# Kernel optimization log

Hardware: AMD Instinct MI355X
Metric: run time of the kernel (lower is better)

The kernel has to match this reference:

```python
import jax, jax.numpy as jnp
import numpy as np

# ---- static config (matches init_kwargs) ----
N, E = 8192, 262144
IN_CH, MP_CH, HID, K = 128, 512, 256, 10
EPS, DELTA = 1e-3, 0.311
TV_COEFF, BAL_COEFF = 0.785, 0.514


def setup_inputs() -> dict:
    key = jax.random.key(0)
    ks = jax.random.split(key, 16)

    def p(k, shape):
        fan_in = shape[0] if len(shape) > 1 else shape[0]
        return (jax.random.normal(k, shape, jnp.float32) / np.sqrt(fan_in)).astype(jnp.float32)

    return {
        "x": jax.random.normal(ks[0], (N, IN_CH), jnp.float32),
        "edge_index": jax.random.randint(ks[1], (2, E), 0, N, jnp.int32),
        "edge_weight": jax.random.uniform(ks[2], (E,), jnp.float32),
        # GTVConv layer 1 / 2 (Linear weight + bias)
        "W1": p(ks[3], (IN_CH, MP_CH)), "b1": jnp.zeros((MP_CH,), jnp.float32),
        "W2": p(ks[4], (MP_CH, MP_CH)), "b2": jnp.zeros((MP_CH,), jnp.float32),
        # pooling MLP [512 -> 256 -> K], relu, no norm
        "Wm1": p(ks[5], (MP_CH, HID)), "bm1": jnp.zeros((HID,), jnp.float32),
        "Wm2": p(ks[6], (HID, K)), "bm2": jnp.zeros((K,), jnp.float32),
    }


def _gtv_conv(x, src, dst, w, W, b):
    """GTVConv: out = elu( h - delta*(D_G h - Gamma h) + b ),
    gamma_ij = w_ij / max(||h_i - h_j||_1, eps), h = x @ W."""
    h = x @ W                                   # [N, C]
    diff = jnp.sum(jnp.abs(h[src] - h[dst]), axis=-1)   # [E]
    gamma = w / jnp.maximum(diff, EPS)                  # [E]
    deg = jnp.zeros(h.shape[0], h.dtype).at[dst].add(gamma)          # [N]
    agg = jnp.zeros_like(h).at[dst].add(gamma[:, None] * h[src])     # Gamma @ h
    out = h - DELTA * (deg[:, None] * h - agg) + b
    return jax.nn.elu(out)


def reference(x, edge_index, edge_weight, W1, b1, W2, b2, Wm1, bm1, Wm2, bm2):
    src, dst = edge_index[0], edge_index[1]

    h = _gtv_conv(x, src, dst, edge_weight, W1, b1)
    h = _gtv_conv(h, src, dst, edge_weight, W2, b2)

    # pooling MLP -> cluster logits s
    s_logits = jax.nn.relu(h @ Wm1 + bm1) @ Wm2 + bm2   # [N, K]

    # dense adjacency (to_dense_adj: duplicate edges accumulate)
    adj = jnp.zeros((N, N), x.dtype).at[src, dst].add(edge_weight)

    s = jax.nn.softmax(s_logits, axis=-1)

    # total-variation loss: sum_ij a_ij * sum_k |s_ik - s_jk| / (2 * nnz(adj))
    tv = jnp.zeros((), x.dtype)
    for k in range(K):  # small fixed loop over clusters, avoids [N,N,K] tensor
        col = s[:, k]
        tv = tv + jnp.sum(adj * jnp.abs(col[:, None] - col[None, :]))
    n_edges = jax.lax.stop_gradient(jnp.count_nonzero(adj).astype(x.dtype))
    tv = tv / (2.0 * n_edges)

    # asymmetric-norm balance loss (AsymCheegerCut)
    idx = N // K + 1                         # rho-quantile index (static)
    quant = jnp.sort(s, axis=0)[N - idx]     # idx-th largest per cluster, [K]
    t = s - quant[None, :]
    asym = jnp.where(t >= 0, (K - 1) * t, -t)
    denom = float(N * (K - 1))
    bal = (denom - jnp.sum(asym)) / denom

    return s_logits, TV_COEFF * tv, BAL_COEFF * bal
```

## Files before the change

kernel.cpp:

```cpp
#include <hip/hip_runtime.h>

#define N_NODES 8192
#define N_EDGES 262144
#define IN_CH 128
#define MP_CH 512
#define HID 256
#define KCL 10
#define EPS_C 0.001f
#define DELTA_C 0.311f
#define TV_COEFF_C 0.785f
#define BAL_COEFF_C 0.514f
#define RANK1 7373
#define DBINS 80


typedef __bf16 bf16x8 __attribute__((ext_vector_type(8)));
typedef float f32x4 __attribute__((ext_vector_type(4)));
typedef unsigned short ushort8 __attribute__((ext_vector_type(8)));

__device__ __forceinline__ float bf2f(unsigned short h) {
  union { unsigned int u; float f; } c; c.u = ((unsigned int)h) << 16; return c.f;
}
__device__ __forceinline__ unsigned short f2bf(float f) {
  union { float f; unsigned int u; } c; c.f = f;
  unsigned int r = c.u + 0x7fffu + ((c.u >> 16) & 1u);
  return (unsigned short)(r >> 16);
}

template <int CTRL, int RMASK>
__device__ __forceinline__ float dpp_add(float x) {
  int d = __builtin_amdgcn_update_dpp(0, __float_as_int(x), CTRL, RMASK, 0xf, true);
  return x + __int_as_float(d);
}
__device__ __forceinline__ float wave_sum64(float x) {
  x = dpp_add<0x111, 0xf>(x);
  x = dpp_add<0x112, 0xf>(x);
  x = dpp_add<0x114, 0xf>(x);
  x = dpp_add<0x118, 0xf>(x);
  x = dpp_add<0x142, 0xa>(x);
  x = dpp_add<0x143, 0xc>(x);
  return __int_as_float(__builtin_amdgcn_readlane(__float_as_int(x), 63));
}

__global__ void prep_kernel(const float* __restrict__ x, const float* __restrict__ W1,
                            const float* __restrict__ W2, const float* __restrict__ Wm1,
                            unsigned short* __restrict__ xb, unsigned short* __restrict__ W1bt,
                            unsigned short* __restrict__ W2bt, unsigned short* __restrict__ Wm1bt,
                            const int* __restrict__ dst, int* __restrict__ cnt) {
  int i = blockIdx.x * 256 + threadIdx.x;
  if (i < 131072) {
    f32x4 a = *(const f32x4*)(x + (size_t)i * 8);
    f32x4 b = *(const f32x4*)(x + (size_t)i * 8 + 4);
    ushort8 ov;
#pragma unroll
    for (int j = 0; j < 4; ++j) { ov[j] = f2bf(a[j]); ov[4 + j] = f2bf(b[j]); }
    *(ushort8*)(xb + (size_t)i * 8) = ov;
    return;
  }
  i -= 131072;
  if (i < 8192) {
    int n = i >> 4, kb = (i & 15) * 8;
    ushort8 ov;
#pragma unroll
    for (int r = 0; r < 8; ++r) ov[r] = f2bf(W1[(size_t)(kb + r) * MP_CH + n]);
    *(ushort8*)(W1bt + (size_t)i * 8) = ov;
    return;
  }
  i -= 8192;
  if (i < 32768) {
    int n = i >> 6, kb = (i & 63) * 8;
    ushort8 ov;
#pragma unroll
    for (int r = 0; r < 8; ++r) ov[r] = f2bf(W2[(size_t)(kb + r) * MP_CH + n]);
    *(ushort8*)(W2bt + (size_t)i * 8) = ov;
    return;
  }
  i -= 32768;
  if (i < 16384) {
    int n = i >> 6, kb = (i & 63) * 8;
    ushort8 ov;
#pragma unroll
    for (int r = 0; r < 8; ++r) ov[r] = f2bf(Wm1[(size_t)(kb + r) * HID + n]);
    *(ushort8*)(Wm1bt + (size_t)i * 8) = ov;
    return;
  }
  i -= 16384;
  if (i < N_EDGES) atomicAdd(&cnt[dst[i]], 1);
}

__global__ __launch_bounds__(1024) void scan_kernel(const int* __restrict__ cnt,
                                                    int* __restrict__ offs,
                                                    int* __restrict__ cursor,
                                                    int* __restrict__ nodeorder) {
  __shared__ int ts[1024];
  __shared__ int dh[DBINS];
  int t = threadIdx.x;
  int v[8]; int s = 0;
#pragma unroll
  for (int j = 0; j < 8; ++j) { v[j] = cnt[t * 8 + j]; s += v[j]; }
  if (t < DBINS) dh[t] = 0;
  ts[t] = s; __syncthreads();
  for (int off = 1; off < 1024; off <<= 1) {
    int add = (t >= off) ? ts[t - off] : 0;
    __syncthreads();
    ts[t] += add;
    __syncthreads();
  }
  int base = ts[t] - s;
#pragma unroll
  for (int j = 0; j < 8; ++j) {
    offs[t * 8 + j] = base; cursor[t * 8 + j] = base; base += v[j];
    int key = v[j] < (DBINS - 1) ? v[j] : (DBINS - 1);
    atomicAdd(&dh[(DBINS - 1) - key], 1);
  }
  if (t == 1023) offs[N_NODES] = ts[1023];
  __syncthreads();
  if (t == 0) {
    int acc0 = 0;
    for (int b = 0; b < DBINS; ++b) { int c = dh[b]; dh[b] = acc0; acc0 += c; }
  }
  __syncthreads();
#pragma unroll
  for (int j = 0; j < 8; ++j) {
    int key = v[j] < (DBINS - 1) ? v[j] : (DBINS - 1);
    int pos = atomicAdd(&dh[(DBINS - 1) - key], 1);
    nodeorder[pos] = t * 8 + j;
  }
}

__global__ void fill_kernel(const int* __restrict__ src, const int* __restrict__ dst,
                            const float* __restrict__ ew, int* __restrict__ cursor,
                            int2* __restrict__ esw, unsigned int* __restrict__ bitmap) {
  for (int e = blockIdx.x * blockDim.x + threadIdx.x; e < N_EDGES; e += gridDim.x * blockDim.x) {
    int a = src[e], b = dst[e];
    float w = ew[e];
    int p = atomicAdd(&cursor[b], 1);
    esw[p] = make_int2(a, __float_as_int(w));
    if (w != 0.f) {
      unsigned int key = ((unsigned int)a << 13) | (unsigned int)b;
      atomicOr(&bitmap[key >> 5], 1u << (key & 31u));
    }
  }
}

__global__ __launch_bounds__(256) void gemm_bt(
    const unsigned short* __restrict__ A, const unsigned short* __restrict__ BT,
    unsigned short* __restrict__ Cb, int N, int K) {
  __shared__ unsigned short lsm[2 * 128 * 32];
  unsigned short* lA = lsm;
  unsigned short* lB = lsm + 128 * 32;
  int lane = threadIdx.x & 63;
  int wv = threadIdx.x >> 6;
  int tm = blockIdx.y * 128, tn = blockIdx.x * 128;
  int wm = (wv >> 1) * 64, wn = (wv & 1) * 64;
  int rA = lane & 15, quad = lane >> 4;
  f32x4 acc[4][4];
#pragma unroll
  for (int i = 0; i < 4; ++i)
#pragma unroll
    for (int j = 0; j < 4; ++j) acc[i][j] = (f32x4){0.f, 0.f, 0.f, 0.f};

  int arow = wv * 32 + (lane >> 2);
  int acol = (lane & 3) * 8;

  for (int k0 = 0; k0 < K; k0 += 32) {
#pragma unroll
    for (int c = 0; c < 2; ++c) {
      const unsigned short* ga = A + (size_t)(tm + arow + c * 16) * K + k0 + acol;
      __builtin_amdgcn_global_load_lds(
          (const __attribute__((address_space(1))) unsigned int*)ga,
          (__attribute__((address_space(3))) unsigned int*)(lA + (wv * 32 + c * 16) * 32),
          16, 0, 0);
      const unsigned short* gb = BT + (size_t)(tn + arow + c * 16) * K + k0 + acol;
      __builtin_amdgcn_global_load_lds(
          (const __attribute__((address_space(1))) unsigned int*)gb,
          (__attribute__((address_space(3))) unsigned int*)(lB + (wv * 32 + c * 16) * 32),
          16, 0, 0);
    }
    __syncthreads();
    bf16x8 af[4], bfr[4];
#pragma unroll
    for (int i = 0; i < 4; ++i)
      af[i] = *(const bf16x8*)(lA + (wm + i * 16 + rA) * 32 + quad * 8);
#pragma unroll
    for (int j = 0; j < 4; ++j)
      bfr[j] = *(const bf16x8*)(lB + (wn + j * 16 + rA) * 32 + quad * 8);
#pragma unroll
    for (int i = 0; i < 4; ++i)
#pragma unroll
      for (int j = 0; j < 4; ++j)
        acc[i][j] = __builtin_amdgcn_mfma_f32_16x16x32_bf16(af[i], bfr[j], acc[i][j], 0, 0, 0);
    __syncthreads();
  }

  float* fbuf = (float*)lsm;
  int band = threadIdx.x >> 7;
  int rrow = (threadIdx.x >> 3) & 15;
  int cg = threadIdx.x & 7;
#pragma unroll
  for (int i = 0; i < 4; ++i) {
#pragma unroll
    for (int j = 0; j < 4; ++j)
#pragma unroll
      for (int r = 0; r < 4; ++r)
        fbuf[(wv >> 1) * (16 * 128) + (quad * 4 + r) * 128 + (wn + j * 16 + rA)] =
            acc[i][j][r];
    __syncthreads();
    const float* sr = fbuf + band * (16 * 128) + rrow * 128 + cg * 16;
    unsigned short ov[16];
#pragma unroll
    for (int c = 0; c < 16; ++c) ov[c] = f2bf(sr[c]);
    size_t gbase = (size_t)(tm + band * 64 + i * 16 + rrow) * N + tn + cg * 16;
    *(ushort8*)(Cb + gbase) = *(ushort8*)ov;
    *(ushort8*)(Cb + gbase + 8) = *(ushort8*)(ov + 8);
    __syncthreads();
  }
}

__global__ __launch_bounds__(256, 8) void gtv_node(
    const unsigned short* __restrict__ hb, const float* __restrict__ bias,
    const int2* __restrict__ esw, const int* __restrict__ offs,
    const int* __restrict__ nodeorder, unsigned short* __restrict__ outb) {
  __shared__ float sacc[2][MP_CH];
  int lane = threadIdx.x & 63;
  int wv = threadIdx.x >> 6;
  int pair = wv >> 1;
  int half = wv & 1;
  int d = __builtin_amdgcn_readfirstlane(nodeorder[blockIdx.x * 2 + pair]);
  ushort8 hdv = ((const ushort8*)(hb + (size_t)d * MP_CH))[lane];
  float hd[8], acc[8];
#pragma unroll
  for (int j = 0; j < 8; ++j) { hd[j] = bf2f(hdv[j]); acc[j] = 0.f; }
  int n0 = offs[d], n1 = offs[d + 1];
  int mid = n0 + ((n1 - n0 + 1) >> 1);
  int e0 = half ? mid : n0;
  int e1 = half ? n1 : mid;
  int i = e0;
  for (; i + 1 < e1; i += 2) {
    int2 ma = esw[i], mb = esw[i + 1];
    float wa = __int_as_float(ma.y), wb = __int_as_float(mb.y);
    ushort8 va = ((const ushort8*)(hb + (size_t)ma.x * MP_CH))[lane];
    ushort8 vb = ((const ushort8*)(hb + (size_t)mb.x * MP_CH))[lane];
    float pa = 0.f, pb = 0.f;
#pragma unroll
    for (int j = 0; j < 8; ++j) {
      pa += fabsf(hd[j] - bf2f(va[j]));
      pb += fabsf(hd[j] - bf2f(vb[j]));
    }
    pa = wave_sum64(pa);
    pb = wave_sum64(pb);
    float ga = wa * __builtin_amdgcn_rcpf(fmaxf(pa, EPS_C));
    float gb = wb * __builtin_amdgcn_rcpf(fmaxf(pb, EPS_C));
#pragma unroll
    for (int j = 0; j < 8; ++j)
      acc[j] += ga * (hd[j] - bf2f(va[j])) + gb * (hd[j] - bf2f(vb[j]));
  }
  if (i < e1) {
    int2 m0 = esw[i];
    float w = __int_as_float(m0.y);
    ushort8 sv = ((const ushort8*)(hb + (size_t)m0.x * MP_CH))[lane];
    float part = 0.f;
#pragma unroll
    for (int j = 0; j < 8; ++j) part += fabsf(hd[j] - bf2f(sv[j]));
    part = wave_sum64(part);
    float g = w * __builtin_amdgcn_rcpf(fmaxf(part, EPS_C));
#pragma unroll
    for (int j = 0; j < 8; ++j) acc[j] += g * (hd[j] - bf2f(sv[j]));
  }
  if (half) {
#pragma unroll
    for (int j = 0; j < 8; ++j) sacc[pair][lane * 8 + j] = acc[j];
  }
  __syncthreads();
  if (!half) {
    const f32x4* br = (const f32x4*)(bias + lane * 8);
    f32x4 b0 = br[0], b1 = br[1];
    unsigned short ov[8];
#pragma unroll
    for (int j = 0; j < 8; ++j) {
      float tot = acc[j] + sacc[pair][lane * 8 + j];
      float bv = (j < 4) ? b0[j] : b1[j - 4];
      float o = hd[j] - DELTA_C * tot + bv;
      o = (o > 0.f) ? o : (expf(o) - 1.f);
      ov[j] = f2bf(o);
    }
    *((ushort8*)(outb + (size_t)d * MP_CH) + lane) = *(ushort8*)ov;
  }
}

__global__ __launch_bounds__(256) void head_fused(
    const unsigned short* __restrict__ A,
    const unsigned short* __restrict__ BT,
    const float* __restrict__ bm1v, const float* __restrict__ Wm2v,
    const float* __restrict__ bm2v, float* __restrict__ out, float* __restrict__ s) {
  __shared__ unsigned short lA[32 * 32];
  __shared__ unsigned short lB[256 * 32];
  __shared__ float hbuf[256 * 41];
  __shared__ float lW2[HID * KCL];
  __shared__ float lb1[HID];
  __shared__ float lb2[KCL];
  int t = threadIdx.x;
  int lane = t & 63, wv = t >> 6;
  int rA = lane & 15, quad = lane >> 4;
  int m0 = blockIdx.x * 32;

  for (int i2 = t; i2 < HID * KCL; i2 += 256) lW2[i2] = Wm2v[i2];
  lb1[t < HID ? t : 0] = bm1v[t < HID ? t : 0];
  if (t < KCL) lb2[t] = bm2v[t];

  f32x4 acc[2][4];
#pragma unroll
  for (int i = 0; i < 2; ++i)
#pragma unroll
    for (int j = 0; j < 4; ++j) acc[i][j] = (f32x4){0.f, 0.f, 0.f, 0.f};

  for (int k0 = 0; k0 < MP_CH; k0 += 32) {
    if (wv < 2) {
      int row = wv * 16 + (lane >> 2);
      const unsigned short* ga = A + (size_t)(m0 + row) * MP_CH + k0 + (lane & 3) * 8;
      __builtin_amdgcn_global_load_lds(
          (const __attribute__((address_space(1))) unsigned int*)ga,
          (__attribute__((address_space(3))) unsigned int*)(lA + (wv * 16) * 32), 16, 0, 0);
    }
#pragma unroll
    for (int q = 0; q < 4; ++q) {
      int idx = wv * 4 + q;
      int row = idx * 16 + (lane >> 2);
      const unsigned short* gb = BT + (size_t)row * MP_CH + k0 + (lane & 3) * 8;
      __builtin_amdgcn_global_load_lds(
          (const __attribute__((address_space(1))) unsigned int*)gb,
          (__attribute__((address_space(3))) unsigned int*)(lB + (idx * 16) * 32), 16, 0, 0);
    }
    __syncthreads();
    bf16x8 af[2], bfr[4];
#pragma unroll
    for (int i = 0; i < 2; ++i)
      af[i] = *(const bf16x8*)(lA + (i * 16 + rA) * 32 + quad * 8);
#pragma unroll
    for (int j = 0; j < 4; ++j)
      bfr[j] = *(const bf16x8*)(lB + (wv * 64 + j * 16 + rA) * 32 + quad * 8);
#pragma unroll
    for (int i = 0; i < 2; ++i)
#pragma unroll
      for (int j = 0; j < 4; ++j)
        acc[i][j] = __builtin_amdgcn_mfma_f32_16x16x32_bf16(af[i], bfr[j], acc[i][j], 0, 0, 0);
    __syncthreads();
  }

#pragma unroll
  for (int i = 0; i < 2; ++i)
#pragma unroll
    for (int j = 0; j < 4; ++j)
#pragma unroll
      for (int r = 0; r < 4; ++r) {
        int row = i * 16 + quad * 4 + r;
        int col = wv * 64 + j * 16 + rA;
        hbuf[col * 41 + row] = fmaxf(acc[i][j][r] + lb1[col], 0.f);
      }
  __syncthreads();

  int row = t >> 3, g = t & 7;
  float p[KCL];
#pragma unroll
  for (int n = 0; n < KCL; ++n) p[n] = 0.f;
#pragma unroll
  for (int k = 0; k < 32; ++k) {
    int col = k * 8 + g;
    float hv = hbuf[col * 41 + row];
    const float* wr = lW2 + col * KCL;
#pragma unroll
    for (int n = 0; n < KCL; ++n) p[n] += hv * wr[n];
  }
#pragma unroll
  for (int n = 0; n < KCL; ++n) {
    p[n] += __shfl_xor(p[n], 1, 64);
    p[n] += __shfl_xor(p[n], 2, 64);
    p[n] += __shfl_xor(p[n], 4, 64);
  }
  if (g == 0) {
    float vv[KCL]; float mx = -1e30f;
    size_t gr = (size_t)(m0 + row);
#pragma unroll
    for (int n = 0; n < KCL; ++n) {
      vv[n] = p[n] + lb2[n];
      out[gr * KCL + n] = vv[n];
      mx = fmaxf(mx, vv[n]);
    }
    float sum = 0.f;
#pragma unroll
    for (int n = 0; n < KCL; ++n) { vv[n] = expf(vv[n] - mx); sum += vv[n]; }
    float inv = 1.f / sum;
#pragma unroll
    for (int n = 0; n < KCL; ++n) s[gr * KCL + n] = vv[n] * inv;
  }
}

__global__ __launch_bounds__(1024) void tvquant_kernel(
    const int* __restrict__ src, const int* __restrict__ dst,
    const float* __restrict__ ew, const float* __restrict__ s,
    const unsigned int* __restrict__ bitmap, float* __restrict__ scal,
    float* __restrict__ out) {
  __shared__ float fsh[16];
  __shared__ int wcnt[2][16];
  __shared__ int psh[16];
  int t = threadIdx.x;
  int lane = t & 63, wv = t >> 6;

  int local_pc = 0;
  {
    const uint4* bm4 = (const uint4*)(bitmap + (size_t)blockIdx.x * 8192);
    uint4 w0 = bm4[t * 2], w1 = bm4[t * 2 + 1];
    local_pc = __popc(w0.x) + __popc(w0.y) + __popc(w0.z) + __popc(w0.w) +
               __popc(w1.x) + __popc(w1.y) + __popc(w1.z) + __popc(w1.w);
  }

  if (blockIdx.x < 246) {
    float local = 0.f;
    for (int e = blockIdx.x * 1024 + t; e < N_EDGES; e += 246 * 1024) {
      int a = src[e], b = dst[e];
      float w = ew[e];
      const float* sa = s + (size_t)a * KCL;
      const float* sb = s + (size_t)b * KCL;
      float tv = 0.f;
#pragma unroll
      for (int k = 0; k < KCL; ++k) tv += fabsf(sa[k] - sb[k]);
      local += w * tv;
    }
#pragma unroll
    for (int m = 1; m < 64; m <<= 1) local += __shfl_xor(local, m, 64);
    if (lane == 0) fsh[wv] = local;
    __syncthreads();
    if (t == 0) {
      float tot = 0.f;
#pragma unroll
      for (int i2 = 0; i2 < 16; ++i2) tot += fsh[i2];
      atomicAdd(&scal[0], tot);
    }
  } else {
    int k = blockIdx.x - 246;
    unsigned int v[8];
#pragma unroll
    for (int j = 0; j < 8; ++j)
      v[j] = __float_as_uint(s[(size_t)(t + j * 1024) * KCL + k]);
    unsigned int lo = 0u, hi = 0x3F800000u;
    int p = 0;
    while (lo < hi) {
      unsigned int mid = (lo + hi) >> 1;
      int c = 0;
#pragma unroll
      for (int j = 0; j < 8; ++j) c += (v[j] <= mid) ? 1 : 0;
#pragma unroll
      for (int m = 1; m < 64; m <<= 1) c += __shfl_xor(c, m, 64);
      if (lane == 0) wcnt[p][wv] = c;
      __syncthreads();
      int tot = 0;
#pragma unroll
      for (int i2 = 0; i2 < 16; ++i2) tot += wcnt[p][i2];
      if (tot >= RANK1) hi = mid; else lo = mid + 1;
      p ^= 1;
    }
    float q = __uint_as_float(lo);
    float local = 0.f;
#pragma unroll
    for (int j = 0; j < 8; ++j) {
      float tt = __uint_as_float(v[j]) - q;
      local += (tt >= 0.f) ? 9.f * tt : -tt;
    }
#pragma unroll
    for (int m = 1; m < 64; m <<= 1) local += __shfl_xor(local, m, 64);
    if (lane == 0) fsh[wv] = local;
    __syncthreads();
    if (t == 0) {
      float tot = 0.f;
#pragma unroll
      for (int i2 = 0; i2 < 16; ++i2) tot += fsh[i2];
      atomicAdd(&scal[1], tot);
    }
  }

#pragma unroll
  for (int m = 1; m < 64; m <<= 1) local_pc += __shfl_xor(local_pc, m, 64);
  if (lane == 0) psh[wv] = local_pc;
  __syncthreads();
  if (t == 0) {
    int tot = 0;
#pragma unroll
    for (int i2 = 0; i2 < 16; ++i2) tot += psh[i2];
    atomicAdd((int*)(scal + 2), tot);
    __threadfence();
    int dn = atomicAdd((int*)(scal + 3), 1);
    if (dn == 255) {
      float tv = atomicAdd(&scal[0], 0.f);
      float asym = atomicAdd(&scal[1], 0.f);
      int ne = atomicAdd((int*)(scal + 2), 0);
      out[N_NODES * KCL] = TV_COEFF_C * (tv / (2.f * (float)ne));
      out[N_NODES * KCL + 1] = BAL_COEFF_C * ((73728.f - asym) / 73728.f);
    }
  }
}

#define OFF_BM     ((size_t)0)
#define OFF_CNT    ((size_t)8388608)
#define OFF_SCAL   ((size_t)8421376)
#define OFF_OFFS   ((size_t)8421888)
#define OFF_CURSOR ((size_t)8454912)
#define OFF_NORD   ((size_t)8487936)
#define OFF_HB     ((size_t)16777216)
#define OFF_OUTB   ((size_t)25165824)
#define OFF_ESW    ((size_t)33554432)
#define OFF_XB     ((size_t)41943040)
#define OFF_W1BT   ((size_t)44040192)
#define OFF_W2BT   ((size_t)44171264)
#define OFF_WM1BT  ((size_t)44695552)
#define OFF_S      ((size_t)44957696)

extern "C" void kernel_launch(void* const* d_in, const int* in_sizes, int n_in,
                              void* d_out, int out_size, void* d_ws, size_t ws_size,
                              hipStream_t stream) {
  const float* x   = (const float*)d_in[0];
  const int*   ei  = (const int*)d_in[1];
  const float* ew  = (const float*)d_in[2];
  const float* W1  = (const float*)d_in[3];
  const float* b1  = (const float*)d_in[4];
  const float* W2  = (const float*)d_in[5];
  const float* b2  = (const float*)d_in[6];
  const float* Wm1 = (const float*)d_in[7];
  const float* bm1 = (const float*)d_in[8];
  const float* Wm2 = (const float*)d_in[9];
  const float* bm2 = (const float*)d_in[10];
  float* out = (float*)d_out;

  char* ws = (char*)d_ws;
  unsigned int*   bitmap = (unsigned int*)(ws + OFF_BM);
  int*            cnt    = (int*)(ws + OFF_CNT);
  float*          scal   = (float*)(ws + OFF_SCAL);
  int*            offs   = (int*)(ws + OFF_OFFS);
  int*            cursor = (int*)(ws + OFF_CURSOR);
  int*            nord   = (int*)(ws + OFF_NORD);
  unsigned short* hb     = (unsigned short*)(ws + OFF_HB);
  unsigned short* outb   = (unsigned short*)(ws + OFF_OUTB);
  int2*           esw    = (int2*)(ws + OFF_ESW);
  unsigned short* xb     = (unsigned short*)(ws + OFF_XB);
  unsigned short* W1bt   = (unsigned short*)(ws + OFF_W1BT);
  unsigned short* W2bt   = (unsigned short*)(ws + OFF_W2BT);
  unsigned short* Wm1bt  = (unsigned short*)(ws + OFF_WM1BT);
  float*          s      = (float*)(ws + OFF_S);

  const int* srcA = ei;
  const int* dstA = ei + N_EDGES;

  hipMemsetAsync(ws, 0, 8421632, stream);

  prep_kernel<<<1760, 256, 0, stream>>>(x, W1, W2, Wm1, xb, W1bt, W2bt, Wm1bt, dstA, cnt);
  scan_kernel<<<1, 1024, 0, stream>>>(cnt, offs, cursor, nord);
  fill_kernel<<<1024, 256, 0, stream>>>(srcA, dstA, ew, cursor, esw, bitmap);

  gemm_bt<<<dim3(MP_CH / 128, N_NODES / 128), 256, 0, stream>>>(xb, W1bt, hb, MP_CH, IN_CH);
  gtv_node<<<N_NODES / 2, 256, 0, stream>>>(hb, b1, esw, offs, nord, outb);
  gemm_bt<<<dim3(MP_CH / 128, N_NODES / 128), 256, 0, stream>>>(outb, W2bt, hb, MP_CH, MP_CH);
  gtv_node<<<N_NODES / 2, 256, 0, stream>>>(hb, b2, esw, offs, nord, outb);
  head_fused<<<N_NODES / 32, 256, 0, stream>>>(outb, Wm1bt, bm1, Wm2, bm2, out, s);

  tvquant_kernel<<<256, 1024, 0, stream>>>(srcA, dstA, ew, s, bitmap, scal, out);
}
```

Before: 254.9 us.

## Restructure GTV node kernel to one wave per node with two-pass channel chunks

The GTV node kernel now gives each node a single wave instead of two half-waves joined through shared memory. Neighbor metadata (up to GCAP=160 edges) is staged in LDS. Pass one computes the L1 distances in four 128-channel chunks, using a 16-lane DPP scan and partial sums in LDS in place of a full 64-lane reduction per edge. Pass two re-gathers the neighbor rows to apply gamma and accumulate. Edges past GCAP fall back to a slow per-edge path, and the extra pass doubles neighbor-row gather traffic and uses narrower 4-byte loads.

```diff
diff --git a/kernel.cpp b/kernel.cpp
--- a/kernel.cpp
+++ b/kernel.cpp
@@ -12,6 +12,7 @@
 #define BAL_COEFF_C 0.514f
 #define RANK1 7373
 #define DBINS 80
+#define GCAP 160
 
 
 typedef __bf16 bf16x8 __attribute__((ext_vector_type(8)));
@@ -40,6 +41,13 @@
   x = dpp_add<0x142, 0xa>(x);
   x = dpp_add<0x143, 0xc>(x);
   return __int_as_float(__builtin_amdgcn_readlane(__float_as_int(x), 63));
+}
+__device__ __forceinline__ float row16_scan(float x) {
+  x = dpp_add<0x111, 0xf>(x);
+  x = dpp_add<0x112, 0xf>(x);
+  x = dpp_add<0x114, 0xf>(x);
+  x = dpp_add<0x118, 0xf>(x);
+  return x;
 }
 
 __global__ void prep_kernel(const float* __restrict__ x, const float* __restrict__ W1,
@@ -221,70 +229,74 @@
     const unsigned short* __restrict__ hb, const float* __restrict__ bias,
     const int2* __restrict__ esw, const int* __restrict__ offs,
     const int* __restrict__ nodeorder, unsigned short* __restrict__ outb) {
-  __shared__ float sacc[2][MP_CH];
+  __shared__ int2 meta[4][GCAP];
+  __shared__ float pd[4][GCAP][4];
   int lane = threadIdx.x & 63;
   int wv = threadIdx.x >> 6;
-  int pair = wv >> 1;
-  int half = wv & 1;
-  int d = __builtin_amdgcn_readfirstlane(nodeorder[blockIdx.x * 2 + pair]);
-  ushort8 hdv = ((const ushort8*)(hb + (size_t)d * MP_CH))[lane];
-  float hd[8], acc[8];
-#pragma unroll
-  for (int j = 0; j < 8; ++j) { hd[j] = bf2f(hdv[j]); acc[j] = 0.f; }
+  int d = __builtin_amdgcn_readfirstlane(nodeorder[blockIdx.x * 4 + wv]);
   int n0 = offs[d], n1 = offs[d + 1];
-  int mid = n0 + ((n1 - n0 + 1) >> 1);
-  int e0 = half ? mid : n0;
-  int e1 = half ? n1 : mid;
-  int i = e0;
-  for (; i + 1 < e1; i += 2) {
-    int2 ma = esw[i], mb = esw[i + 1];
-    float wa = __int_as_float(ma.y), wb = __int_as_float(mb.y);
-    ushort8 va = ((const ushort8*)(hb + (size_t)ma.x * MP_CH))[lane];
-    ushort8 vb = ((const ushort8*)(hb + (size_t)mb.x * MP_CH))[lane];
-    float pa = 0.f, pb = 0.f;
-#pragma unroll
-    for (int j = 0; j < 8; ++j) {
-      pa += fabsf(hd[j] - bf2f(va[j]));
-      pb += fabsf(hd[j] - bf2f(vb[j]));
-    }
-    pa = wave_sum64(pa);
-    pb = wave_sum64(pb);
-    float ga = wa * __builtin_amdgcn_rcpf(fmaxf(pa, EPS_C));
-    float gb = wb * __builtin_amdgcn_rcpf(fmaxf(pb, EPS_C));
-#pragma unroll
-    for (int j = 0; j < 8; ++j)
-      acc[j] += ga * (hd[j] - bf2f(va[j])) + gb * (hd[j] - bf2f(vb[j]));
-  }
-  if (i < e1) {
-    int2 m0 = esw[i];
-    float w = __int_as_float(m0.y);
-    ushort8 sv = ((const ushort8*)(hb + (size_t)m0.x * MP_CH))[lane];
-    float part = 0.f;
-#pragma unroll
-    for (int j = 0; j < 8; ++j) part += fabsf(hd[j] - bf2f(sv[j]));
-    part = wave_sum64(part);
-    float g = w * __builtin_amdgcn_rcpf(fmaxf(part, EPS_C));
-#pragma unroll
-    for (int j = 0; j < 8; ++j) acc[j] += g * (hd[j] - bf2f(sv[j]));
-  }
-  if (half) {
-#pragma unroll
-    for (int j = 0; j < 8; ++j) sacc[pair][lane * 8 + j] = acc[j];
-  }
-  __syncthreads();
-  if (!half) {
-    const f32x4* br = (const f32x4*)(bias + lane * 8);
-    f32x4 b0 = br[0], b1 = br[1];
-    unsigned short ov[8];
-#pragma unroll
-    for (int j = 0; j < 8; ++j) {
-      float tot = acc[j] + sacc[pair][lane * 8 + j];
-      float bv = (j < 4) ? b0[j] : b1[j - 4];
-      float o = hd[j] - DELTA_C * tot + bv;
-      o = (o > 0.f) ? o : (expf(o) - 1.f);
-      ov[j] = f2bf(o);
-    }
-    *((ushort8*)(outb + (size_t)d * MP_CH) + lane) = *(ushort8*)ov;
+  int ne = n1 - n0;
+  int nf = ne < GCAP ? ne : GCAP;
+
+  for (int e = lane; e < nf; e += 64) {
+    meta[wv][e] = esw[n0 + e];
+    pd[wv][e][0] = 0.f; pd[wv][e][1] = 0.f; pd[wv][e][2] = 0.f; pd[wv][e][3] = 0.f;
+  }
+
+  for (int c = 0; c < 4; ++c) {
+    const unsigned short* hbase = hb + c * 128 + lane * 2;
+    unsigned int hu = *(const unsigned int*)(hbase + (size_t)d * MP_CH);
+    float h0 = bf2f((unsigned short)(hu & 0xffffu));
+    float h1 = bf2f((unsigned short)(hu >> 16));
+    for (int e = 0; e < nf; ++e) {
+      int src = meta[wv][e].x;
+      unsigned int vu = *(const unsigned int*)(hbase + (size_t)src * MP_CH);
+      float p = fabsf(h0 - bf2f((unsigned short)(vu & 0xffffu))) +
+                fabsf(h1 - bf2f((unsigned short)(vu >> 16)));
+      p = row16_scan(p);
+      if ((lane & 15) == 15) pd[wv][e][lane >> 4] += p;
+    }
+  }
+
+  for (int e = lane; e < nf; e += 64) {
+    float dist = pd[wv][e][0] + pd[wv][e][1] + pd[wv][e][2] + pd[wv][e][3];
+    float w = __int_as_float(meta[wv][e].y);
+    pd[wv][e][0] = w * __builtin_amdgcn_rcpf(fmaxf(dist, EPS_C));
+  }
+
+  for (int c = 0; c < 4; ++c) {
+    const unsigned short* hbase = hb + c * 128 + lane * 2;
+    unsigned int hu = *(const unsigned int*)(hbase + (size_t)d * MP_CH);
+    float h0 = bf2f((unsigned short)(hu & 0xffffu));
+    float h1 = bf2f((unsigned short)(hu >> 16));
+    float a0 = 0.f, a1 = 0.f;
+    for (int e = 0; e < nf; ++e) {
+      int src = meta[wv][e].x;
+      float g = pd[wv][e][0];
+      unsigned int vu = *(const unsigned int*)(hbase + (size_t)src * MP_CH);
+      a0 += g * (h0 - bf2f((unsigned short)(vu & 0xffffu)));
+      a1 += g * (h1 - bf2f((unsigned short)(vu >> 16)));
+    }
+    for (int e = GCAP; e < ne; ++e) {
+      int2 m = esw[n0 + e];
+      ushort8 dv = ((const ushort8*)(hb + (size_t)d * MP_CH))[lane];
+      ushort8 sv = ((const ushort8*)(hb + (size_t)m.x * MP_CH))[lane];
+      float part = 0.f;
+#pragma unroll
+      for (int j = 0; j < 8; ++j) part += fabsf(bf2f(dv[j]) - bf2f(sv[j]));
+      part = wave_sum64(part);
+      float g = __int_as_float(m.y) * __builtin_amdgcn_rcpf(fmaxf(part, EPS_C));
+      unsigned int vu = *(const unsigned int*)(hbase + (size_t)m.x * MP_CH);
+      a0 += g * (h0 - bf2f((unsigned short)(vu & 0xffffu)));
+      a1 += g * (h1 - bf2f((unsigned short)(vu >> 16)));
+    }
+    float2 bv = *(const float2*)(bias + c * 128 + lane * 2);
+    float o0 = h0 - DELTA_C * a0 + bv.x;
+    float o1 = h1 - DELTA_C * a1 + bv.y;
+    o0 = (o0 > 0.f) ? o0 : (expf(o0) - 1.f);
+    o1 = (o1 > 0.f) ? o1 : (expf(o1) - 1.f);
+    unsigned int ou = (unsigned int)f2bf(o0) | ((unsigned int)f2bf(o1) << 16);
+    *(unsigned int*)(outb + (size_t)d * MP_CH + c * 128 + lane * 2) = ou;
   }
 }
 
@@ -556,9 +568,9 @@
   fill_kernel<<<1024, 256, 0, stream>>>(srcA, dstA, ew, cursor, esw, bitmap);
 
   gemm_bt<<<dim3(MP_CH / 128, N_NODES / 128), 256, 0, stream>>>(xb, W1bt, hb, MP_CH, IN_CH);
-  gtv_node<<<N_NODES / 2, 256, 0, stream>>>(hb, b1, esw, offs, nord, outb);
+  gtv_node<<<N_NODES / 4, 256, 0, stream>>>(hb, b1, esw, offs, nord, outb);
   gemm_bt<<<dim3(MP_CH / 128, N_NODES / 128), 256, 0, stream>>>(outb, W2bt, hb, MP_CH, MP_CH);
-  gtv_node<<<N_NODES / 2, 256, 0, stream>>>(hb, b2, esw, offs, nord, outb);
+  gtv_node<<<N_NODES / 4, 256, 0, stream>>>(hb, b2, esw, offs, nord, outb);
   head_fused<<<N_NODES / 32, 256, 0, stream>>>(outb, Wm1bt, bm1, Wm2, bm2, out, s);
 
   tvquant_kernel<<<256, 1024, 0, stream>>>(srcA, dstA, ew, s, bitmap, scal, out);
```

After: 386.9 us. +51.8%, slower.
